# Optimization experiments

Measured on AMD Instinct MI355X. Metric: run time of the kernel, lower is better.

## Reference

```python
import jax, jax.numpy as jnp
import numpy as np

VOCAB = 29
VEC = 512      # vector_dim
HID = 1024     # hidden_size
SEN = 64       # sen_len (== seq length)
BATCH = 2048


def setup_inputs() -> dict:
    key = jax.random.key(0)
    k1, k2, k3, k4, k5, k6 = jax.random.split(key, 6)
    s_emb = 1.0
    s_ih = 1.0 / np.sqrt(HID)
    s_cls = 1.0 / np.sqrt(HID)
    return {
        "x": jax.random.randint(k1, (BATCH, SEN), 0, VOCAB, dtype=jnp.int64),
        "emb": jax.random.normal(k2, (VOCAB, VEC), dtype=jnp.float32) * s_emb,
        "W_ih": jax.random.uniform(k3, (HID, VEC), dtype=jnp.float32, minval=-s_ih, maxval=s_ih),
        "W_hh": jax.random.uniform(k4, (HID, HID), dtype=jnp.float32, minval=-s_ih, maxval=s_ih),
        "W_cls": jax.random.uniform(k5, (SEN + 1, HID), dtype=jnp.float32, minval=-s_cls, maxval=s_cls),
        "b_cls": jax.random.uniform(k6, (SEN + 1,), dtype=jnp.float32, minval=-s_cls, maxval=s_cls),
    }


def reference(x, emb, W_ih, W_hh, W_cls, b_cls):
    # Embedding lookup: [B, S, VEC]
    xe = emb[x]
    # Precompute input projections for all timesteps: [B, S, HID]
    xin = jnp.einsum("bsv,hv->bsh", xe, W_ih)

    def step(h, x_t):
        # h: [B, HID], x_t: [B, HID] (already W_ih @ x)
        h_new = jnp.tanh(x_t + h @ W_hh.T)
        return h_new, None

    h0 = jnp.zeros((x.shape[0], HID), dtype=xin.dtype)
    h_last, _ = jax.lax.scan(step, h0, jnp.swapaxes(xin, 0, 1))  # scan over S

    # h.squeeze() in torch (num_layers=1) -> [B, HID]
    logits = h_last @ W_cls.T + b_cls  # [B, SEN+1]
    return logits
```

## Files before the change

### kernel.cpp

```cpp
#include <hip/hip_runtime.h>
#include <hip/hip_bf16.h>

#define VOCAB 29
#define VEC   512
#define HID   1024
#define SEN   64
#define BATCH 2048

typedef __bf16 bf16_t;
typedef bf16_t bf16x8 __attribute__((ext_vector_type(8)));
typedef float  floatx4 __attribute__((ext_vector_type(4)));

__global__ void cvt_whh(const float* __restrict__ w, bf16_t* __restrict__ o, int n) {
    int i = blockIdx.x * blockDim.x + threadIdx.x;
    if (i < n) o[i] = (bf16_t)w[i];
}

__global__ void cvt_wcls(const float* __restrict__ w, bf16_t* __restrict__ o) {
    int i = blockIdx.x * blockDim.x + threadIdx.x;
    if (i >= 80 * HID) return;
    o[i] = (i < 65 * HID) ? (bf16_t)w[i] : (bf16_t)0.0f;
}

__global__ void proj_kernel(const float* __restrict__ emb, const float* __restrict__ wih,
                            float* __restrict__ proj) {
    int idx = blockIdx.x * blockDim.x + threadIdx.x;
    if (idx >= VOCAB * HID) return;
    int v = idx / HID, h = idx % HID;
    const float* e = emb + v * VEC;
    const float* w = wih + h * VEC;
    float s = 0.f;
    for (int k = 0; k < VEC; k += 4) {
        float4 ev = *(const float4*)(e + k);
        float4 wv = *(const float4*)(w + k);
        s += ev.x * wv.x + ev.y * wv.y + ev.z * wv.z + ev.w * wv.w;
    }
    proj[idx] = s;
}

__device__ __forceinline__ float fast_tanh(float x) {
    float e = __expf(2.0f * x);
    return 1.0f - 2.0f / (e + 1.0f);
}

__device__ __forceinline__ void load16_to_lds(const bf16_t* g, bf16_t* l) {
    auto gp = reinterpret_cast<const __attribute__((address_space(1))) unsigned int*>(
        reinterpret_cast<uintptr_t>(g));
    auto lp = reinterpret_cast<__attribute__((address_space(3))) unsigned int*>(
        static_cast<unsigned int>(reinterpret_cast<uintptr_t>(l)));
    __builtin_amdgcn_global_load_lds(gp, lp, 16, 0, 0);
}

__device__ __forceinline__ int flag_ld(const int* p) {
    return __hip_atomic_load(p, __ATOMIC_RELAXED, __HIP_MEMORY_SCOPE_AGENT);
}

#define BM 128
#define BN 64
#define PANEL_BLKS 16
#define SB() __builtin_amdgcn_sched_barrier(0)

#define LOAD_G(B, G) {                                               \
    const int c0_ = 2 * (G);                                         \
    afb[B][0] = *(const bf16x8*)(hA + c0_ * 32);                     \
    afb[B][1] = *(const bf16x8*)(hA + 16 * HID + c0_ * 32);          \
    afb[B][2] = *(const bf16x8*)(hA + (c0_ + 1) * 32);               \
    afb[B][3] = *(const bf16x8*)(hA + 16 * HID + (c0_ + 1) * 32); }

#define COMP_G(B, G)                                                 \
    _Pragma("unroll")                                                \
    for (int j = 0; j < 2; j++) {                                    \
        const int c_ = 2 * (G) + j;                                  \
        const int p_ = ((4 * c_ + q) ^ l7) * 8;                      \
        bf16x8 b0 = *(const bf16x8*)&Bsh[l16][p_];                   \
        bf16x8 b1 = *(const bf16x8*)&Bsh[16 + l16][p_];              \
        bf16x8 b2 = *(const bf16x8*)&Bsh[32 + l16][p_];              \
        bf16x8 b3 = *(const bf16x8*)&Bsh[48 + l16][p_];              \
        bf16x8 a0 = afb[B][2 * j], a1 = afb[B][2 * j + 1];           \
        acc[0][0] = __builtin_amdgcn_mfma_f32_16x16x32_bf16(a0, b0, acc[0][0], 0, 0, 0); \
        acc[0][1] = __builtin_amdgcn_mfma_f32_16x16x32_bf16(a0, b1, acc[0][1], 0, 0, 0); \
        acc[0][2] = __builtin_amdgcn_mfma_f32_16x16x32_bf16(a0, b2, acc[0][2], 0, 0, 0); \
        acc[0][3] = __builtin_amdgcn_mfma_f32_16x16x32_bf16(a0, b3, acc[0][3], 0, 0, 0); \
        acc[1][0] = __builtin_amdgcn_mfma_f32_16x16x32_bf16(a1, b0, acc[1][0], 0, 0, 0); \
        acc[1][1] = __builtin_amdgcn_mfma_f32_16x16x32_bf16(a1, b1, acc[1][1], 0, 0, 0); \
        acc[1][2] = __builtin_amdgcn_mfma_f32_16x16x32_bf16(a1, b2, acc[1][2], 0, 0, 0); \
        acc[1][3] = __builtin_amdgcn_mfma_f32_16x16x32_bf16(a1, b3, acc[1][3], 0, 0, 0); \
    }

__global__ __launch_bounds__(256, 1)
void rnn_persist(const bf16_t* __restrict__ whh, const float* __restrict__ proj,
                 const int* __restrict__ x, bf16_t* hbuf, int* scnt)
{
    __shared__ __align__(16) bf16_t Bsh[BN][HID];
    __shared__ int uni_sh;

    const int tid  = threadIdx.x;
    const int bx   = blockIdx.x, by = blockIdx.y;
    const int m0   = bx * BM;
    const int n0   = by * BN;
    const int wave = tid >> 6;
    const int lane = tid & 63;
    const int wm   = wave * 32;
    const int q    = lane >> 4;
    const int l16  = lane & 15;
    const int l7   = l16 & 7;

    int* cnt   = scnt + bx * 64;
    int* xmask = scnt + (16 + bx) * 64;
    int* fl    = scnt + (32 + bx) * 64;

#pragma unroll
    for (int half = 0; half < 2; half++)
#pragma unroll
        for (int it = 0; it < 16; it++) {
            const int r = it * 4 + wave;
            load16_to_lds(whh + (n0 + r) * HID + half * 512 + (lane ^ (r & 7)) * 8,
                          &Bsh[r][half * 512 + lane * 8]);
        }

    int rowl[8];
#pragma unroll
    for (int mi = 0; mi < 2; mi++)
#pragma unroll
        for (int r = 0; r < 4; r++) rowl[mi * 4 + r] = m0 + wm + mi * 16 + q * 4 + r;

    {
        float pv0[8][4];
#pragma unroll
        for (int i = 0; i < 8; i++) {
            const int tok = x[rowl[i] * SEN + 0];
            const float* pr = proj + tok * HID + n0;
#pragma unroll
            for (int ni = 0; ni < 4; ni++) pv0[i][ni] = pr[ni * 16 + l16];
        }
#pragma unroll
        for (int i = 0; i < 8; i++)
#pragma unroll
            for (int ni = 0; ni < 4; ni++)
                hbuf[rowl[i] * HID + n0 + ni * 16 + l16] = (bf16_t)fast_tanh(pv0[i][ni]);
    }

    int tk[8];
#pragma unroll
    for (int i = 0; i < 8; i++) tk[i] = x[rowl[i] * SEN + 1];

    __syncthreads();
    if (tid == 0) {
        __hip_atomic_store(&fl[by], 1, __ATOMIC_RELAXED, __HIP_MEMORY_SCOPE_AGENT);
        const int my_xcd = (int)__builtin_amdgcn_s_getreg((3 << 11) | 20);
        __hip_atomic_fetch_or(xmask, 1 << my_xcd, __ATOMIC_RELAXED, __HIP_MEMORY_SCOPE_AGENT);
        __hip_atomic_fetch_add(cnt, 1, __ATOMIC_RELEASE, __HIP_MEMORY_SCOPE_AGENT);
        while (__hip_atomic_load(cnt, __ATOMIC_ACQUIRE, __HIP_MEMORY_SCOPE_AGENT) < PANEL_BLKS)
            __builtin_amdgcn_s_sleep(1);
        const int m = __hip_atomic_load(xmask, __ATOMIC_RELAXED, __HIP_MEMORY_SCOPE_AGENT);
        uni_sh = ((m & (m - 1)) == 0);
    }
    __syncthreads();
    asm volatile("buffer_inv" ::: "memory");
    const int fast = uni_sh;

#pragma unroll 1
    for (int t = 1; t < SEN; t++) {
        const bf16_t* h_in  = hbuf + (size_t)((t + 1) & 1) * (BATCH * HID);
        bf16_t*       h_out = hbuf + (size_t)(t & 1) * (BATCH * HID);

        floatx4 acc[2][4];
#pragma unroll
        for (int i = 0; i < 2; i++)
#pragma unroll
            for (int j = 0; j < 4; j++) acc[i][j] = (floatx4){0.f, 0.f, 0.f, 0.f};

        const bf16_t* hA = h_in + (m0 + wm + l16) * HID + q * 8;
        bf16x8 afb[2][4];

        LOAD_G(0, by)
        {
            const int g1 = (by + 1) & 15;
            if (fast) { while (flag_ld(&fl[g1]) < t) {} }
            LOAD_G(1, g1)
        }
        float pv[8][4];
#pragma unroll
        for (int i = 0; i < 8; i++) {
            const float* pr = proj + tk[i] * HID + n0;
#pragma unroll
            for (int ni = 0; ni < 4; ni++) pv[i][ni] = pr[ni * 16 + l16];
        }

#pragma unroll
        for (int i = 0; i < 16; i++) {
            const int g   = (by + i) & 15;
            const int gn2 = (by + i + 2) & 15;
            int fv = t;
            if (i < 14 && fast) fv = flag_ld(&fl[gn2]);
            SB();
            COMP_G(i & 1, g)
            SB();
            if (i < 14) {
                if (fast) { while (fv < t) fv = flag_ld(&fl[gn2]); }
                LOAD_G(i & 1, gn2)
            }
            if (i == 13 && t < SEN - 1) {
#pragma unroll
                for (int ii = 0; ii < 8; ii++) tk[ii] = x[rowl[ii] * SEN + t + 1];
            }
        }

#pragma unroll
        for (int mi = 0; mi < 2; mi++)
#pragma unroll
            for (int r = 0; r < 4; r++)
#pragma unroll
                for (int ni = 0; ni < 4; ni++) {
                    float v = acc[mi][ni][r] + pv[mi * 4 + r][ni];
                    h_out[rowl[mi * 4 + r] * HID + n0 + ni * 16 + l16] = (bf16_t)fast_tanh(v);
                }

        if (t < SEN - 1) {
            __syncthreads();
            if (fast) {
                if (tid == 0)
                    __hip_atomic_store(&fl[by], t + 1,
                                       __ATOMIC_RELAXED, __HIP_MEMORY_SCOPE_AGENT);
            } else {
                if (tid == 0) {
                    __hip_atomic_fetch_add(cnt, 1, __ATOMIC_RELEASE, __HIP_MEMORY_SCOPE_AGENT);
                    while (__hip_atomic_load(cnt, __ATOMIC_ACQUIRE, __HIP_MEMORY_SCOPE_AGENT)
                           < PANEL_BLKS * (t + 1))
                        __builtin_amdgcn_s_sleep(1);
                }
                __syncthreads();
            }
            asm volatile("buffer_inv" ::: "memory");
        }
    }
}

#undef LOAD_G
#undef COMP_G

#define CBM 128
#define CLDK 72
__global__ __launch_bounds__(256)
void classifier_mfma(const bf16_t* __restrict__ h, const bf16_t* __restrict__ wcls,
                     const float* __restrict__ bcls, float* __restrict__ out)
{
    __shared__ __align__(16) bf16_t Ash[CBM][CLDK];
    __shared__ __align__(16) bf16_t Bsh[80][CLDK];

    const int tid = threadIdx.x;
    const int m0 = blockIdx.x * CBM;
    const int wave = tid >> 6, lane = tid & 63;
    const int wm = wave * 32;
    const int q = lane >> 4, l16 = lane & 15;

    floatx4 acc[2][5];
#pragma unroll
    for (int i = 0; i < 2; i++)
#pragma unroll
        for (int j = 0; j < 5; j++) acc[i][j] = (floatx4){0.f, 0.f, 0.f, 0.f};

    for (int kk = 0; kk < HID; kk += 64) {
#pragma unroll
        for (int it = 0; it < 4; it++) {
            int idx = tid + it * 256, r = idx >> 3, c = (idx & 7) * 8;
            *(uint4*)&Ash[r][c] = *(const uint4*)&h[(m0 + r) * HID + kk + c];
        }
#pragma unroll
        for (int it = 0; it < 3; it++) {
            int idx = tid + it * 256;
            if (idx < 640) {
                int r = idx >> 3, c = (idx & 7) * 8;
                *(uint4*)&Bsh[r][c] = *(const uint4*)&wcls[r * HID + kk + c];
            }
        }
        __syncthreads();
#pragma unroll
        for (int ks = 0; ks < 64; ks += 32) {
            bf16x8 af[2], bfr[5];
#pragma unroll
            for (int mi = 0; mi < 2; mi++)
                af[mi] = *(const bf16x8*)&Ash[wm + mi * 16 + l16][ks + q * 8];
#pragma unroll
            for (int ni = 0; ni < 5; ni++)
                bfr[ni] = *(const bf16x8*)&Bsh[ni * 16 + l16][ks + q * 8];
#pragma unroll
            for (int mi = 0; mi < 2; mi++)
#pragma unroll
                for (int ni = 0; ni < 5; ni++)
                    acc[mi][ni] = __builtin_amdgcn_mfma_f32_16x16x32_bf16(
                        af[mi], bfr[ni], acc[mi][ni], 0, 0, 0);
        }
        __syncthreads();
    }

#pragma unroll
    for (int mi = 0; mi < 2; mi++) {
#pragma unroll
        for (int r = 0; r < 4; r++) {
            int gm = m0 + wm + mi * 16 + q * 4 + r;
#pragma unroll
            for (int ni = 0; ni < 5; ni++) {
                int gn = ni * 16 + l16;
                if (gn < SEN + 1)
                    out[gm * (SEN + 1) + gn] = acc[mi][ni][r] + bcls[gn];
            }
        }
    }
}

extern "C" void kernel_launch(void* const* d_in, const int* in_sizes, int n_in,
                              void* d_out, int out_size, void* d_ws, size_t ws_size,
                              hipStream_t stream)
{
    const int*   x     = (const int*)  d_in[0];
    const float* emb   = (const float*)d_in[1];
    const float* w_ih  = (const float*)d_in[2];
    const float* w_hh  = (const float*)d_in[3];
    const float* w_cls = (const float*)d_in[4];
    const float* b_cls = (const float*)d_in[5];
    float* out = (float*)d_out;

    char* ws = (char*)d_ws;
    bf16_t* whh_bf  = (bf16_t*)ws;
    float*  proj    = (float*)(ws + (2u << 20));
    bf16_t* wcls_bf = (bf16_t*)(ws + (2u << 20) + (128u << 10));
    bf16_t* h0      = (bf16_t*)(ws + (2u << 20) + (288u << 10));
    bf16_t* h1      = (bf16_t*)(ws + (6u << 20) + (288u << 10));
    int*    scnt    = (int*)   (ws + (10u << 20) + (288u << 10));

    hipMemsetAsync(scnt, 0, 16384, stream);
    cvt_whh<<<(HID * HID) / 256, 256, 0, stream>>>(w_hh, whh_bf, HID * HID);
    proj_kernel<<<(VOCAB * HID + 255) / 256, 256, 0, stream>>>(emb, w_ih, proj);
    cvt_wcls<<<(80 * HID) / 256, 256, 0, stream>>>(w_cls, wcls_bf);

    dim3 grid(BATCH / BM, HID / BN);
    rnn_persist<<<grid, 256, 0, stream>>>(whh_bf, proj, x, h0, scnt);

    classifier_mfma<<<BATCH / CBM, 256, 0, stream>>>(h1, wcls_bf, b_cls, out);
}
```

Measured before the change: 858.4 us.

## Use 8 waves per block and replace per-group flags with panel barrier

The persistent RNN block grows from 4 to 8 waves, each owning 16 rows instead of 32. That halves per-wave MFMA work and register use and allows up to 2 blocks per CU. The fine-grained per-column-group flag polling, which let a block start consuming h chunks as soon as they were ready, is replaced by a full panel counter barrier at every timestep. The A loads now use a fixed 4-deep prefetch ring instead of the rotated order. The trade-off is more latency parallelism and simpler loads, but the block can no longer overlap its compute with slower peer blocks.

```diff
diff --git a/kernel.cpp b/kernel.cpp
--- a/kernel.cpp
+++ b/kernel.cpp
@@ -51,10 +51,6 @@
     __builtin_amdgcn_global_load_lds(gp, lp, 16, 0, 0);
 }
 
-__device__ __forceinline__ int flag_ld(const int* p) {
-    return __hip_atomic_load(p, __ATOMIC_RELAXED, __HIP_MEMORY_SCOPE_AGENT);
-}
-
 #define BM 128
 #define BN 64
 #define PANEL_BLKS 16
@@ -63,9 +59,7 @@
 #define LOAD_G(B, G) {                                               \
     const int c0_ = 2 * (G);                                         \
     afb[B][0] = *(const bf16x8*)(hA + c0_ * 32);                     \
-    afb[B][1] = *(const bf16x8*)(hA + 16 * HID + c0_ * 32);          \
-    afb[B][2] = *(const bf16x8*)(hA + (c0_ + 1) * 32);               \
-    afb[B][3] = *(const bf16x8*)(hA + 16 * HID + (c0_ + 1) * 32); }
+    afb[B][1] = *(const bf16x8*)(hA + (c0_ + 1) * 32); }
 
 #define COMP_G(B, G)                                                 \
     _Pragma("unroll")                                                \
@@ -76,18 +70,14 @@
         bf16x8 b1 = *(const bf16x8*)&Bsh[16 + l16][p_];              \
         bf16x8 b2 = *(const bf16x8*)&Bsh[32 + l16][p_];              \
         bf16x8 b3 = *(const bf16x8*)&Bsh[48 + l16][p_];              \
-        bf16x8 a0 = afb[B][2 * j], a1 = afb[B][2 * j + 1];           \
-        acc[0][0] = __builtin_amdgcn_mfma_f32_16x16x32_bf16(a0, b0, acc[0][0], 0, 0, 0); \
-        acc[0][1] = __builtin_amdgcn_mfma_f32_16x16x32_bf16(a0, b1, acc[0][1], 0, 0, 0); \
-        acc[0][2] = __builtin_amdgcn_mfma_f32_16x16x32_bf16(a0, b2, acc[0][2], 0, 0, 0); \
-        acc[0][3] = __builtin_amdgcn_mfma_f32_16x16x32_bf16(a0, b3, acc[0][3], 0, 0, 0); \
-        acc[1][0] = __builtin_amdgcn_mfma_f32_16x16x32_bf16(a1, b0, acc[1][0], 0, 0, 0); \
-        acc[1][1] = __builtin_amdgcn_mfma_f32_16x16x32_bf16(a1, b1, acc[1][1], 0, 0, 0); \
-        acc[1][2] = __builtin_amdgcn_mfma_f32_16x16x32_bf16(a1, b2, acc[1][2], 0, 0, 0); \
-        acc[1][3] = __builtin_amdgcn_mfma_f32_16x16x32_bf16(a1, b3, acc[1][3], 0, 0, 0); \
-    }
-
-__global__ __launch_bounds__(256, 1)
+        bf16x8 a0 = afb[B][j];                                       \
+        acc[0] = __builtin_amdgcn_mfma_f32_16x16x32_bf16(a0, b0, acc[0], 0, 0, 0); \
+        acc[1] = __builtin_amdgcn_mfma_f32_16x16x32_bf16(a0, b1, acc[1], 0, 0, 0); \
+        acc[2] = __builtin_amdgcn_mfma_f32_16x16x32_bf16(a0, b2, acc[2], 0, 0, 0); \
+        acc[3] = __builtin_amdgcn_mfma_f32_16x16x32_bf16(a0, b3, acc[3], 0, 0, 0); \
+    }
+
+__global__ __launch_bounds__(512, 2)
 void rnn_persist(const bf16_t* __restrict__ whh, const float* __restrict__ proj,
                  const int* __restrict__ x, bf16_t* hbuf, int* scnt)
 {
@@ -100,53 +90,49 @@
     const int n0   = by * BN;
     const int wave = tid >> 6;
     const int lane = tid & 63;
-    const int wm   = wave * 32;
+    const int wm   = wave * 16;
     const int q    = lane >> 4;
     const int l16  = lane & 15;
     const int l7   = l16 & 7;
 
     int* cnt   = scnt + bx * 64;
     int* xmask = scnt + (16 + bx) * 64;
-    int* fl    = scnt + (32 + bx) * 64;
 
 #pragma unroll
     for (int half = 0; half < 2; half++)
 #pragma unroll
-        for (int it = 0; it < 16; it++) {
-            const int r = it * 4 + wave;
+        for (int it = 0; it < 8; it++) {
+            const int r = it * 8 + wave;
             load16_to_lds(whh + (n0 + r) * HID + half * 512 + (lane ^ (r & 7)) * 8,
                           &Bsh[r][half * 512 + lane * 8]);
         }
 
-    int rowl[8];
-#pragma unroll
-    for (int mi = 0; mi < 2; mi++)
-#pragma unroll
-        for (int r = 0; r < 4; r++) rowl[mi * 4 + r] = m0 + wm + mi * 16 + q * 4 + r;
+    int rowl[4];
+#pragma unroll
+    for (int r = 0; r < 4; r++) rowl[r] = m0 + wm + q * 4 + r;
 
     {
-        float pv0[8][4];
-#pragma unroll
-        for (int i = 0; i < 8; i++) {
+        float pv0[4][4];
+#pragma unroll
+        for (int i = 0; i < 4; i++) {
             const int tok = x[rowl[i] * SEN + 0];
             const float* pr = proj + tok * HID + n0;
 #pragma unroll
             for (int ni = 0; ni < 4; ni++) pv0[i][ni] = pr[ni * 16 + l16];
         }
 #pragma unroll
-        for (int i = 0; i < 8; i++)
+        for (int i = 0; i < 4; i++)
 #pragma unroll
             for (int ni = 0; ni < 4; ni++)
                 hbuf[rowl[i] * HID + n0 + ni * 16 + l16] = (bf16_t)fast_tanh(pv0[i][ni]);
     }
 
-    int tk[8];
-#pragma unroll
-    for (int i = 0; i < 8; i++) tk[i] = x[rowl[i] * SEN + 1];
+    int tk[4];
+#pragma unroll
+    for (int i = 0; i < 4; i++) tk[i] = x[rowl[i] * SEN + 1];
 
     __syncthreads();
     if (tid == 0) {
-        __hip_atomic_store(&fl[by], 1, __ATOMIC_RELAXED, __HIP_MEMORY_SCOPE_AGENT);
         const int my_xcd = (int)__builtin_amdgcn_s_getreg((3 << 11) | 20);
         __hip_atomic_fetch_or(xmask, 1 << my_xcd, __ATOMIC_RELAXED, __HIP_MEMORY_SCOPE_AGENT);
         __hip_atomic_fetch_add(cnt, 1, __ATOMIC_RELEASE, __HIP_MEMORY_SCOPE_AGENT);
@@ -164,64 +150,52 @@
         const bf16_t* h_in  = hbuf + (size_t)((t + 1) & 1) * (BATCH * HID);
         bf16_t*       h_out = hbuf + (size_t)(t & 1) * (BATCH * HID);
 
-        floatx4 acc[2][4];
-#pragma unroll
-        for (int i = 0; i < 2; i++)
-#pragma unroll
-            for (int j = 0; j < 4; j++) acc[i][j] = (floatx4){0.f, 0.f, 0.f, 0.f};
+        floatx4 acc[4];
+#pragma unroll
+        for (int j = 0; j < 4; j++) acc[j] = (floatx4){0.f, 0.f, 0.f, 0.f};
 
         const bf16_t* hA = h_in + (m0 + wm + l16) * HID + q * 8;
-        bf16x8 afb[2][4];
-
-        LOAD_G(0, by)
-        {
-            const int g1 = (by + 1) & 15;
-            if (fast) { while (flag_ld(&fl[g1]) < t) {} }
-            LOAD_G(1, g1)
-        }
-        float pv[8][4];
-#pragma unroll
-        for (int i = 0; i < 8; i++) {
+        bf16x8 afb[4][2];
+
+        LOAD_G(0, 0) LOAD_G(1, 1) LOAD_G(2, 2) LOAD_G(3, 3)
+
+        float pv[4][4];
+#pragma unroll
+        for (int i = 0; i < 4; i++) {
             const float* pr = proj + tk[i] * HID + n0;
 #pragma unroll
             for (int ni = 0; ni < 4; ni++) pv[i][ni] = pr[ni * 16 + l16];
         }
+        SB();
 
 #pragma unroll
         for (int i = 0; i < 16; i++) {
-            const int g   = (by + i) & 15;
-            const int gn2 = (by + i + 2) & 15;
-            int fv = t;
-            if (i < 14 && fast) fv = flag_ld(&fl[gn2]);
+            COMP_G(i & 3, i)
+            if (i < 12) { LOAD_G(i & 3, i + 4) }
+            if (i == 12 && t < SEN - 1) {
+#pragma unroll
+                for (int ii = 0; ii < 4; ii++) tk[ii] = x[rowl[ii] * SEN + t + 1];
+            }
             SB();
-            COMP_G(i & 1, g)
-            SB();
-            if (i < 14) {
-                if (fast) { while (fv < t) fv = flag_ld(&fl[gn2]); }
-                LOAD_G(i & 1, gn2)
-            }
-            if (i == 13 && t < SEN - 1) {
-#pragma unroll
-                for (int ii = 0; ii < 8; ii++) tk[ii] = x[rowl[ii] * SEN + t + 1];
-            }
-        }
-
-#pragma unroll
-        for (int mi = 0; mi < 2; mi++)
-#pragma unroll
-            for (int r = 0; r < 4; r++)
-#pragma unroll
-                for (int ni = 0; ni < 4; ni++) {
-                    float v = acc[mi][ni][r] + pv[mi * 4 + r][ni];
-                    h_out[rowl[mi * 4 + r] * HID + n0 + ni * 16 + l16] = (bf16_t)fast_tanh(v);
-                }
+        }
+
+#pragma unroll
+        for (int r = 0; r < 4; r++)
+#pragma unroll
+            for (int ni = 0; ni < 4; ni++) {
+                float v = acc[ni][r] + pv[r][ni];
+                h_out[rowl[r] * HID + n0 + ni * 16 + l16] = (bf16_t)fast_tanh(v);
+            }
 
         if (t < SEN - 1) {
             __syncthreads();
             if (fast) {
-                if (tid == 0)
-                    __hip_atomic_store(&fl[by], t + 1,
-                                       __ATOMIC_RELAXED, __HIP_MEMORY_SCOPE_AGENT);
+                if (tid == 0) {
+                    __hip_atomic_fetch_add(cnt, 1, __ATOMIC_RELAXED, __HIP_MEMORY_SCOPE_AGENT);
+                    while (__hip_atomic_load(cnt, __ATOMIC_RELAXED, __HIP_MEMORY_SCOPE_AGENT)
+                           < PANEL_BLKS * (t + 1))
+                        __builtin_amdgcn_s_sleep(1);
+                }
             } else {
                 if (tid == 0) {
                     __hip_atomic_fetch_add(cnt, 1, __ATOMIC_RELEASE, __HIP_MEMORY_SCOPE_AGENT);
@@ -229,8 +203,8 @@
                            < PANEL_BLKS * (t + 1))
                         __builtin_amdgcn_s_sleep(1);
                 }
-                __syncthreads();
-            }
+            }
+            __syncthreads();
             asm volatile("buffer_inv" ::: "memory");
         }
     }
@@ -335,7 +309,7 @@
     cvt_wcls<<<(80 * HID) / 256, 256, 0, stream>>>(w_cls, wcls_bf);
 
     dim3 grid(BATCH / BM, HID / BN);
-    rnn_persist<<<grid, 256, 0, stream>>>(whh_bf, proj, x, h0, scnt);
+    rnn_persist<<<grid, 512, 0, stream>>>(whh_bf, proj, x, h0, scnt);
 
     classifier_mfma<<<BATCH / CBM, 256, 0, stream>>>(h1, wcls_bf, b_cls, out);
 }
```

Result: faster. 709.8 us (-17.3%).
